# Kernel tuning notes

Hardware: AMD Instinct MI355X
Metric: run time of the kernel (lower is better)

Reference implementation:

```python
import jax, jax.numpy as jnp
import numpy as np

# model hyperparameters (from init_kwargs 'model' mapping)
SIG = 10.0       # kernel length scale
C = 0.0          # energy integration constant
STD = 1.0        # normalization std
M, N_ATOMS = 64, 24
T_ROWS, DESC = 6000, N_ATOMS * (N_ATOMS - 1) // 2  # 276


def setup_inputs() -> dict:
    key = jax.random.key(0)
    k1, k2, k3 = jax.random.split(key, 3)
    # spread atoms out so pairwise distances are O(1..10) Angstrom-like
    Rs = jax.random.normal(k1, (M, N_ATOMS, 3), jnp.float32) * 3.0
    # training descriptors are inverse distances -> positive values in (0,1)
    xs_train = jax.random.uniform(k2, (T_ROWS, DESC), jnp.float32)
    Jx_alphas = jax.random.normal(k3, (T_ROWS, DESC), jnp.float32) * 0.1
    return {"Rs": Rs, "xs_train": xs_train, "Jx_alphas": Jx_alphas}


def reference(Rs, xs_train, Jx_alphas):
    sig = SIG
    q = np.sqrt(5.0) / sig
    m, n = Rs.shape[0], Rs.shape[1]
    i, j = np.tril_indices(n, k=-1)  # lower-triangular atom pairs, P entries

    # pairwise coordinate differences [M, N, N, 3]
    diffs = Rs[:, :, None, :] - Rs[:, None, :, :]
    # inverse pairwise distances over tril pairs -> descriptor xs [M, P]
    d_ij = jnp.linalg.norm(diffs[:, i, j, :], axis=-1)
    xs = 1.0 / d_ij

    # descriptor differences to all (permuted) training points [M, T, P]
    x_diffs = q * xs[:, None, :] - q * xs_train[None, :, :]
    x_dists = jnp.linalg.norm(x_diffs, axis=-1)            # [M, T]
    exp_xs = (5.0 / (3.0 * sig ** 2)) * jnp.exp(-x_dists)  # [M, T]
    dot = jnp.einsum('mtp,tp->mt', x_diffs, Jx_alphas)     # [M, T]
    exp1 = exp_xs * (1.0 + x_dists)                        # [M, T]

    F1 = jnp.einsum('mt,mtp->mp', exp_xs * dot, x_diffs)   # [M, P]
    F2 = exp1 @ Jx_alphas                                  # [M, P]
    Fs_x = (F1 - F2) * xs ** 3                             # [M, P]

    # scatter pair forces back onto the symmetric [N, N] pair grid;
    # diagonal diffs are zero so leaving mult=0 there matches the original
    mult = jnp.zeros((m, n, n), Rs.dtype)
    mult = mult.at[:, i, j].set(Fs_x).at[:, j, i].set(Fs_x)
    Fs = (diffs * mult[..., None]).sum(axis=1) * STD       # [M, N, 3]

    Es = (exp1 * dot).sum(axis=-1) / q * STD + C           # [M]
    return Es, Fs
```

## Files before the change

kernel.cpp:

```cpp
#include <hip/hip_runtime.h>
#include <math.h>

#define MM 64
#define NA 24
#define NP 276
#define NT 6000
#define QC 0.22360679774997896f
#define EXPC 0.01666666666666667f

#define OFF_XS   0
#define OFF_UU   17664
#define OFF_VV   17728
#define OFF_C1   23728
#define OFF_ES   29728
#define OFF_SW   29792
#define OFF_SH   29856
#define OFF_WT   312480
#define OFF_ET   696480
#define ZTOT     282752

__device__ __forceinline__ float f4c(const float4& v, int i) {
  return i == 0 ? v.x : i == 1 ? v.y : i == 2 ? v.z : v.w;
}

__global__ __launch_bounds__(256) void k_pre(const float* __restrict__ Rs,
                                             const float* __restrict__ xt,
                                             const float* __restrict__ Ja,
                                             float* __restrict__ ws) {
  const int tid = threadIdx.x;
  for (int z = blockIdx.x * 256 + tid; z < ZTOT; z += gridDim.x * 256)
    ws[OFF_ES + z] = 0.f;

  if (blockIdx.x < MM) {
    const int m = blockIdx.x;
    __shared__ float sR[NA * 3];
    __shared__ float sAcc[4];
    if (tid < NA * 3) sR[tid] = Rs[m * NA * 3 + tid];
    __syncthreads();
    float acc = 0.f;
    for (int p = tid; p < NP; p += 256) {
      int i = (int)((1.0f + sqrtf(1.0f + 8.0f * (float)p)) * 0.5f);
      while (i * (i - 1) / 2 > p) i--;
      while ((i + 1) * i / 2 <= p) i++;
      int j = p - i * (i - 1) / 2;
      float dx = sR[i * 3 + 0] - sR[j * 3 + 0];
      float dy = sR[i * 3 + 1] - sR[j * 3 + 1];
      float dz = sR[i * 3 + 2] - sR[j * 3 + 2];
      float u = 1.0f / sqrtf(dx * dx + dy * dy + dz * dz);
      ws[OFF_XS + m * NP + p] = u;
      acc += u * u;
    }
    for (int off = 32; off; off >>= 1) acc += __shfl_down(acc, off);
    if ((tid & 63) == 0) sAcc[tid >> 6] = acc;
    __syncthreads();
    if (tid == 0) ws[OFF_UU + m] = sAcc[0] + sAcc[1] + sAcc[2] + sAcc[3];
  } else {
    const int t = (blockIdx.x - MM) * 4 + (tid >> 6);
    const int lane = tid & 63;
    if (t < NT) {
      const float* vrow = xt + (size_t)t * NP;
      const float* jrow = Ja + (size_t)t * NP;
      float a = 0.f, b = 0.f;
      for (int p = lane; p < NP; p += 64) {
        float v = vrow[p], j = jrow[p];
        a += v * v;
        b += v * j;
      }
      for (int off = 32; off; off >>= 1) {
        a += __shfl_down(a, off);
        b += __shfl_down(b, off);
      }
      if (lane == 0) { ws[OFF_VV + t] = a; ws[OFF_C1 + t] = b; }
    }
  }
}

#define G1_BS 278
__global__ __launch_bounds__(128) void k_g1(const float* __restrict__ xt,
                                            const float* __restrict__ Ja,
                                            float* __restrict__ ws) {
  __shared__ __align__(16) float2 Bs[16][G1_BS];
  const int tid = threadIdx.x;
  const int t0 = blockIdx.x * 16;
  const int my = blockIdx.y * 16;
  for (int idx = tid; idx < 16 * 69; idx += 128) {
    const int row = idx / 69;
    const int k = (idx - row * 69) * 4;
    const float4 v = *(const float4*)(xt + (size_t)(t0 + row) * NP + k);
    const float4 j = *(const float4*)(Ja + (size_t)(t0 + row) * NP + k);
    *(float4*)&Bs[row][k]     = make_float4(v.x, j.x, v.y, j.y);
    *(float4*)&Bs[row][k + 2] = make_float4(v.z, j.z, v.w, j.w);
  }
  const int r = tid >> 3;
  const int c = tid & 7;
  const int m = my + r;
  const float uum = ws[OFF_UU + m];
  const float2 vv2 = *(const float2*)(ws + OFF_VV + t0 + 2 * c);
  const float2 c12 = *(const float2*)(ws + OFF_C1 + t0 + 2 * c);
  const float* arow = ws + OFF_XS + m * NP;
  __syncthreads();

  float accv0 = 0.f, accj0 = 0.f, accv1 = 0.f, accj1 = 0.f;
#pragma unroll 3
  for (int k = 0; k < NP; k += 4) {
    const float4 a = *(const float4*)(arow + k);
    const float4 p00 = *(const float4*)&Bs[2 * c][k];
    const float4 p01 = *(const float4*)&Bs[2 * c][k + 2];
    const float4 p10 = *(const float4*)&Bs[2 * c + 1][k];
    const float4 p11 = *(const float4*)&Bs[2 * c + 1][k + 2];
    accv0 = fmaf(a.x, p00.x, accv0); accj0 = fmaf(a.x, p00.y, accj0);
    accv0 = fmaf(a.y, p00.z, accv0); accj0 = fmaf(a.y, p00.w, accj0);
    accv0 = fmaf(a.z, p01.x, accv0); accj0 = fmaf(a.z, p01.y, accj0);
    accv0 = fmaf(a.w, p01.z, accv0); accj0 = fmaf(a.w, p01.w, accj0);
    accv1 = fmaf(a.x, p10.x, accv1); accj1 = fmaf(a.x, p10.y, accj1);
    accv1 = fmaf(a.y, p10.z, accv1); accj1 = fmaf(a.y, p10.w, accj1);
    accv1 = fmaf(a.z, p11.x, accv1); accj1 = fmaf(a.z, p11.y, accj1);
    accv1 = fmaf(a.w, p11.z, accv1); accj1 = fmaf(a.w, p11.w, accj1);
  }

  float es_p = 0.f, sw_p = 0.f;
#pragma unroll
  for (int tt = 0; tt < 2; tt++) {
    const float g1v = tt ? accv1 : accv0;
    const float g2v = tt ? accj1 : accj0;
    const float vvt = tt ? vv2.y : vv2.x;
    const float c1t = tt ? c12.y : c12.x;
    float d2 = fmaxf(uum - 2.f * g1v + vvt, 0.f);
    float xd = QC * sqrtf(d2);
    float dv = QC * (g2v - c1t);
    float ex = EXPC * __expf(-xd);
    float e1v = ex * (1.f + xd);
    float w_ = ex * dv;
    const int t = t0 + 2 * c + tt;
    ws[OFF_WT + (size_t)t * 64 + m] = w_;
    ws[OFF_ET + (size_t)t * 64 + m] = e1v;
    es_p += e1v * dv;
    sw_p += w_;
  }
#pragma unroll
  for (int off = 4; off; off >>= 1) {
    es_p += __shfl_down(es_p, off);
    sw_p += __shfl_down(sw_p, off);
  }
  if (c == 0) {
    atomicAdd(ws + OFF_ES + m, es_p);
    atomicAdd(ws + OFF_SW + m, sw_p);
  }
}

#define G2_KC 125
__global__ __launch_bounds__(256) void k_g2(const float* __restrict__ xt,
                                            const float* __restrict__ Ja,
                                            float* __restrict__ ws) {
  __shared__ __align__(16) float Bsv[G2_KC][16];
  __shared__ __align__(16) float Bsj[G2_KC][16];
  const int tid = threadIdx.x;
  const int p0 = blockIdx.x * 16;
  const int k0 = blockIdx.y * G2_KC;
  const int validp = (NP - p0 < 16) ? (NP - p0) : 16;

  for (int idx = tid; idx < G2_KC * 8; idx += 256) {
    const int q = idx & 3;
    const int mat = (idx >> 2) & 1;
    const int row = idx >> 3;
    float4 val = make_float4(0.f, 0.f, 0.f, 0.f);
    if (q * 4 < validp)
      val = *(const float4*)((mat ? Ja : xt) + (size_t)(k0 + row) * NP + p0 + q * 4);
    *(float4*)&(mat ? Bsj : Bsv)[row][q * 4] = val;
  }
  __syncthreads();

  const int m = tid & 63;
  const int pg = tid >> 6;
  const float* wtp = ws + OFF_WT + (size_t)k0 * 64 + m;
  const float* etp = ws + OFF_ET + (size_t)k0 * 64 + m;
  float acc1[4] = {0.f, 0.f, 0.f, 0.f};
  float acc2[4] = {0.f, 0.f, 0.f, 0.f};

#pragma unroll 5
  for (int k = 0; k < G2_KC; k++) {
    const float aw = wtp[k * 64];
    const float ae = etp[k * 64];
    const float4 bv = *(const float4*)&Bsv[k][pg * 4];
    const float4 bj = *(const float4*)&Bsj[k][pg * 4];
    acc1[0] = fmaf(aw, bv.x, acc1[0]); acc2[0] = fmaf(ae, bj.x, acc2[0]);
    acc1[1] = fmaf(aw, bv.y, acc1[1]); acc2[1] = fmaf(ae, bj.y, acc2[1]);
    acc1[2] = fmaf(aw, bv.z, acc1[2]); acc2[2] = fmaf(ae, bj.z, acc2[2]);
    acc1[3] = fmaf(aw, bv.w, acc1[3]); acc2[3] = fmaf(ae, bj.w, acc2[3]);
  }

  const int sh = blockIdx.y & 7;
  float* base1 = ws + OFF_SH + (size_t)(sh * 2 + 0) * NP * 64;
  float* base2 = ws + OFF_SH + (size_t)(sh * 2 + 1) * NP * 64;
#pragma unroll
  for (int j = 0; j < 4; j++) {
    const int p = p0 + pg * 4 + j;
    if (p < NP && pg * 4 + j < validp) {
      atomicAdd(base1 + (size_t)p * 64 + m, acc1[j]);
      atomicAdd(base2 + (size_t)p * 64 + m, acc2[j]);
    }
  }
}

__global__ __launch_bounds__(320) void k_final(const float* __restrict__ Rs,
                                               const float* __restrict__ ws,
                                               float* __restrict__ out) {
  const int m = blockIdx.x;
  const int tid = threadIdx.x;
  __shared__ float fx[NP];
  __shared__ float sR[NA * 3];
  if (tid < NA * 3) sR[tid] = Rs[m * NA * 3 + tid];
  const float sw = ws[OFF_SW + m];
  for (int p = tid; p < NP; p += 320) {
    float f1p = 0.f, f2 = 0.f;
#pragma unroll
    for (int s = 0; s < 8; s++) {
      f1p += ws[OFF_SH + ((size_t)(s * 2 + 0) * NP + p) * 64 + m];
      f2  += ws[OFF_SH + ((size_t)(s * 2 + 1) * NP + p) * 64 + m];
    }
    const float u = ws[OFF_XS + m * NP + p];
    const float F1 = QC * (u * sw - f1p);
    fx[p] = (F1 - f2) * u * u * u;
  }
  __syncthreads();
  if (tid == 0) out[m] = ws[OFF_ES + m] / QC;
  if (tid < NA * 3) {
    const int a = tid / 3, cc = tid % 3;
    const float ra = sR[a * 3 + cc];
    float acc = 0.f;
    for (int b = 0; b < NA; b++) {
      if (b == a) continue;
      const int i = a > b ? a : b, j = a > b ? b : a;
      const int p = i * (i - 1) / 2 + j;
      acc += (sR[b * 3 + cc] - ra) * fx[p];
    }
    out[MM + m * NA * 3 + tid] = acc;
  }
}

extern "C" void kernel_launch(void* const* d_in, const int* in_sizes, int n_in,
                              void* d_out, int out_size, void* d_ws, size_t ws_size,
                              hipStream_t stream) {
  const float* Rs = (const float*)d_in[0];
  const float* xt = (const float*)d_in[1];
  const float* Ja = (const float*)d_in[2];
  float* out = (float*)d_out;
  float* ws = (float*)d_ws;

  k_pre<<<MM + NT / 4, 256, 0, stream>>>(Rs, xt, Ja, ws);
  k_g1<<<dim3(NT / 16, 4), 128, 0, stream>>>(xt, Ja, ws);
  k_g2<<<dim3(18, NT / G2_KC), 256, 0, stream>>>(xt, Ja, ws);
  k_final<<<MM, 320, 0, stream>>>(Rs, ws, out);
}
```

Measured before the change: 138.5 us.

## Transpose training data into interleaved p-major layout and restructure first GEMM

The preprocessing kernel now transposes xs_train and Jx_alphas into a p-major workspace buffer with interleaved (x, J) pairs, and stores the query descriptors p-major as well. The first distance/dot kernel is rewritten so each thread owns one training row and eight molecules, streaming coalesced float2 loads over p instead of staging tiles in shared memory. This is meant to remove the shared-memory tile loads and give coalesced global access with more register reuse. The cost is an extra full write and read of a transposed copy of the training data, plus fewer, smaller blocks in the first GEMM.

```diff
diff --git a/kernel.cpp b/kernel.cpp
--- a/kernel.cpp
+++ b/kernel.cpp
@@ -5,10 +5,11 @@
 #define NA 24
 #define NP 276
 #define NT 6000
+#define NTP 6016
 #define QC 0.22360679774997896f
 #define EXPC 0.01666666666666667f
 
-#define OFF_XS   0
+#define OFF_XST  0
 #define OFF_UU   17664
 #define OFF_VV   17728
 #define OFF_C1   23728
@@ -17,6 +18,7 @@
 #define OFF_SH   29856
 #define OFF_WT   312480
 #define OFF_ET   696480
+#define OFF_XJT  1080480
 #define ZTOT     282752
 
 __device__ __forceinline__ float f4c(const float4& v, int i) {
@@ -47,7 +49,7 @@
       float dy = sR[i * 3 + 1] - sR[j * 3 + 1];
       float dz = sR[i * 3 + 2] - sR[j * 3 + 2];
       float u = 1.0f / sqrtf(dx * dx + dy * dy + dz * dz);
-      ws[OFF_XS + m * NP + p] = u;
+      ws[OFF_XST + p * 64 + m] = u;
       acc += u * u;
     }
     for (int off = 32; off; off >>= 1) acc += __shfl_down(acc, off);
@@ -55,96 +57,123 @@
     __syncthreads();
     if (tid == 0) ws[OFF_UU + m] = sAcc[0] + sAcc[1] + sAcc[2] + sAcc[3];
   } else {
-    const int t = (blockIdx.x - MM) * 4 + (tid >> 6);
-    const int lane = tid & 63;
-    if (t < NT) {
-      const float* vrow = xt + (size_t)t * NP;
-      const float* jrow = Ja + (size_t)t * NP;
-      float a = 0.f, b = 0.f;
-      for (int p = lane; p < NP; p += 64) {
-        float v = vrow[p], j = jrow[p];
-        a += v * v;
-        b += v * j;
-      }
-      for (int off = 32; off; off >>= 1) {
-        a += __shfl_down(a, off);
-        b += __shfl_down(b, off);
-      }
-      if (lane == 0) { ws[OFF_VV + t] = a; ws[OFF_C1 + t] = b; }
-    }
-  }
-}
-
-#define G1_BS 278
-__global__ __launch_bounds__(128) void k_g1(const float* __restrict__ xt,
-                                            const float* __restrict__ Ja,
-                                            float* __restrict__ ws) {
-  __shared__ __align__(16) float2 Bs[16][G1_BS];
-  const int tid = threadIdx.x;
-  const int t0 = blockIdx.x * 16;
-  const int my = blockIdx.y * 16;
-  for (int idx = tid; idx < 16 * 69; idx += 128) {
-    const int row = idx / 69;
-    const int k = (idx - row * 69) * 4;
-    const float4 v = *(const float4*)(xt + (size_t)(t0 + row) * NP + k);
-    const float4 j = *(const float4*)(Ja + (size_t)(t0 + row) * NP + k);
-    *(float4*)&Bs[row][k]     = make_float4(v.x, j.x, v.y, j.y);
-    *(float4*)&Bs[row][k + 2] = make_float4(v.z, j.z, v.w, j.w);
-  }
-  const int r = tid >> 3;
-  const int c = tid & 7;
-  const int m = my + r;
-  const float uum = ws[OFF_UU + m];
-  const float2 vv2 = *(const float2*)(ws + OFF_VV + t0 + 2 * c);
-  const float2 c12 = *(const float2*)(ws + OFF_C1 + t0 + 2 * c);
-  const float* arow = ws + OFF_XS + m * NP;
-  __syncthreads();
-
-  float accv0 = 0.f, accj0 = 0.f, accv1 = 0.f, accj1 = 0.f;
-#pragma unroll 3
-  for (int k = 0; k < NP; k += 4) {
-    const float4 a = *(const float4*)(arow + k);
-    const float4 p00 = *(const float4*)&Bs[2 * c][k];
-    const float4 p01 = *(const float4*)&Bs[2 * c][k + 2];
-    const float4 p10 = *(const float4*)&Bs[2 * c + 1][k];
-    const float4 p11 = *(const float4*)&Bs[2 * c + 1][k + 2];
-    accv0 = fmaf(a.x, p00.x, accv0); accj0 = fmaf(a.x, p00.y, accj0);
-    accv0 = fmaf(a.y, p00.z, accv0); accj0 = fmaf(a.y, p00.w, accj0);
-    accv0 = fmaf(a.z, p01.x, accv0); accj0 = fmaf(a.z, p01.y, accj0);
-    accv0 = fmaf(a.w, p01.z, accv0); accj0 = fmaf(a.w, p01.w, accj0);
-    accv1 = fmaf(a.x, p10.x, accv1); accj1 = fmaf(a.x, p10.y, accj1);
-    accv1 = fmaf(a.y, p10.z, accv1); accj1 = fmaf(a.y, p10.w, accj1);
-    accv1 = fmaf(a.z, p11.x, accv1); accj1 = fmaf(a.z, p11.y, accj1);
-    accv1 = fmaf(a.w, p11.z, accv1); accj1 = fmaf(a.w, p11.w, accj1);
-  }
-
-  float es_p = 0.f, sw_p = 0.f;
-#pragma unroll
-  for (int tt = 0; tt < 2; tt++) {
-    const float g1v = tt ? accv1 : accv0;
-    const float g2v = tt ? accj1 : accj0;
-    const float vvt = tt ? vv2.y : vv2.x;
-    const float c1t = tt ? c12.y : c12.x;
-    float d2 = fmaxf(uum - 2.f * g1v + vvt, 0.f);
+    const int t0 = (blockIdx.x - MM) * 32;
+    const int tl = tid >> 5;
+    const int pl = tid & 31;
+    __shared__ float lx[32][33];
+    __shared__ float lj[32][33];
+    float vvp[4] = {0.f, 0.f, 0.f, 0.f};
+    float c1p[4] = {0.f, 0.f, 0.f, 0.f};
+    for (int c9 = 0; c9 < 9; c9++) {
+      const int p = c9 * 32 + pl;
+      const bool pok = (p < NP);
+      __syncthreads();
+#pragma unroll
+      for (int tt = 0; tt < 4; tt++) {
+        const int t = t0 + tl * 4 + tt;
+        float v = 0.f, j = 0.f;
+        if (pok && t < NT) {
+          v = xt[(size_t)t * NP + p];
+          j = Ja[(size_t)t * NP + p];
+        }
+        vvp[tt] += v * v;
+        c1p[tt] += v * j;
+        lx[pl][tl * 4 + tt] = v;
+        lj[pl][tl * 4 + tt] = j;
+      }
+      __syncthreads();
+      const int tlw = tid & 31;
+      const int plw = tid >> 5;
+#pragma unroll
+      for (int pp = 0; pp < 4; pp++) {
+        const int pLoc = plw * 4 + pp;
+        const int pOut = c9 * 32 + pLoc;
+        if (pOut < NP) {
+          *(float2*)(ws + OFF_XJT + ((size_t)pOut * NTP + t0 + tlw) * 2) =
+              make_float2(lx[pLoc][tlw], lj[pLoc][tlw]);
+        }
+      }
+    }
+#pragma unroll
+    for (int off = 16; off; off >>= 1) {
+#pragma unroll
+      for (int tt = 0; tt < 4; tt++) {
+        vvp[tt] += __shfl_down(vvp[tt], off, 32);
+        c1p[tt] += __shfl_down(c1p[tt], off, 32);
+      }
+    }
+    if (pl == 0) {
+#pragma unroll
+      for (int tt = 0; tt < 4; tt++) {
+        const int t = t0 + tl * 4 + tt;
+        if (t < NT) { ws[OFF_VV + t] = vvp[tt]; ws[OFF_C1 + t] = c1p[tt]; }
+      }
+    }
+  }
+}
+
+__global__ __launch_bounds__(64) void k_g1(float* __restrict__ ws) {
+  const int lane = threadIdx.x;
+  const int t = blockIdx.x * 64 + lane;
+  const int m0 = blockIdx.y * 8;
+  const float* __restrict__ xj = ws + OFF_XJT + (size_t)t * 2;
+  const float* __restrict__ xs = ws + OFF_XST + m0;
+  float av[8] = {0.f,0.f,0.f,0.f,0.f,0.f,0.f,0.f};
+  float aj[8] = {0.f,0.f,0.f,0.f,0.f,0.f,0.f,0.f};
+#pragma unroll 4
+  for (int p = 0; p < NP; p++) {
+    const float2 x = *(const float2*)(xj + (size_t)p * (NTP * 2));
+    const float4 a0 = *(const float4*)(xs + p * 64);
+    const float4 a1 = *(const float4*)(xs + p * 64 + 4);
+    av[0] = fmaf(a0.x, x.x, av[0]); aj[0] = fmaf(a0.x, x.y, aj[0]);
+    av[1] = fmaf(a0.y, x.x, av[1]); aj[1] = fmaf(a0.y, x.y, aj[1]);
+    av[2] = fmaf(a0.z, x.x, av[2]); aj[2] = fmaf(a0.z, x.y, aj[2]);
+    av[3] = fmaf(a0.w, x.x, av[3]); aj[3] = fmaf(a0.w, x.y, aj[3]);
+    av[4] = fmaf(a1.x, x.x, av[4]); aj[4] = fmaf(a1.x, x.y, aj[4]);
+    av[5] = fmaf(a1.y, x.x, av[5]); aj[5] = fmaf(a1.y, x.y, aj[5]);
+    av[6] = fmaf(a1.z, x.x, av[6]); aj[6] = fmaf(a1.z, x.y, aj[6]);
+    av[7] = fmaf(a1.w, x.x, av[7]); aj[7] = fmaf(a1.w, x.y, aj[7]);
+  }
+  const bool tok = (t < NT);
+  const float vvt = tok ? ws[OFF_VV + t] : 0.f;
+  const float c1t = tok ? ws[OFF_C1 + t] : 0.f;
+  float wv[8], ev[8], es8[8], sw8[8];
+#pragma unroll
+  for (int i = 0; i < 8; i++) {
+    const float uum = ws[OFF_UU + m0 + i];
+    float d2 = fmaxf(uum - 2.f * av[i] + vvt, 0.f);
     float xd = QC * sqrtf(d2);
-    float dv = QC * (g2v - c1t);
+    float dv = QC * (aj[i] - c1t);
     float ex = EXPC * __expf(-xd);
     float e1v = ex * (1.f + xd);
     float w_ = ex * dv;
-    const int t = t0 + 2 * c + tt;
-    ws[OFF_WT + (size_t)t * 64 + m] = w_;
-    ws[OFF_ET + (size_t)t * 64 + m] = e1v;
-    es_p += e1v * dv;
-    sw_p += w_;
-  }
-#pragma unroll
-  for (int off = 4; off; off >>= 1) {
-    es_p += __shfl_down(es_p, off);
-    sw_p += __shfl_down(sw_p, off);
-  }
-  if (c == 0) {
-    atomicAdd(ws + OFF_ES + m, es_p);
-    atomicAdd(ws + OFF_SW + m, sw_p);
+    if (!tok) { e1v = 0.f; w_ = 0.f; dv = 0.f; }
+    wv[i] = w_; ev[i] = e1v;
+    es8[i] = e1v * dv;
+    sw8[i] = w_;
+  }
+  if (tok) {
+    float* wp = ws + OFF_WT + (size_t)t * 64 + m0;
+    float* ep = ws + OFF_ET + (size_t)t * 64 + m0;
+    *(float4*)wp       = make_float4(wv[0], wv[1], wv[2], wv[3]);
+    *(float4*)(wp + 4) = make_float4(wv[4], wv[5], wv[6], wv[7]);
+    *(float4*)ep       = make_float4(ev[0], ev[1], ev[2], ev[3]);
+    *(float4*)(ep + 4) = make_float4(ev[4], ev[5], ev[6], ev[7]);
+  }
+#pragma unroll
+  for (int off = 32; off; off >>= 1) {
+#pragma unroll
+    for (int i = 0; i < 8; i++) {
+      es8[i] += __shfl_down(es8[i], off);
+      sw8[i] += __shfl_down(sw8[i], off);
+    }
+  }
+  if (lane == 0) {
+#pragma unroll
+    for (int i = 0; i < 8; i++) {
+      atomicAdd(ws + OFF_ES + m0 + i, es8[i]);
+      atomicAdd(ws + OFF_SW + m0 + i, sw8[i]);
+    }
   }
 }
 
@@ -218,7 +247,7 @@
       f1p += ws[OFF_SH + ((size_t)(s * 2 + 0) * NP + p) * 64 + m];
       f2  += ws[OFF_SH + ((size_t)(s * 2 + 1) * NP + p) * 64 + m];
     }
-    const float u = ws[OFF_XS + m * NP + p];
+    const float u = ws[OFF_XST + p * 64 + m];
     const float F1 = QC * (u * sw - f1p);
     fx[p] = (F1 - f2) * u * u * u;
   }
@@ -247,8 +276,8 @@
   float* out = (float*)d_out;
   float* ws = (float*)d_ws;
 
-  k_pre<<<MM + NT / 4, 256, 0, stream>>>(Rs, xt, Ja, ws);
-  k_g1<<<dim3(NT / 16, 4), 128, 0, stream>>>(xt, Ja, ws);
+  k_pre<<<MM + 188, 256, 0, stream>>>(Rs, xt, Ja, ws);
+  k_g1<<<dim3(94, 8), 64, 0, stream>>>(ws);
   k_g2<<<dim3(18, NT / G2_KC), 256, 0, stream>>>(xt, Ja, ws);
   k_final<<<MM, 320, 0, stream>>>(Rs, ws, out);
 }
```

Result: slower. 175.5 us (+26.7%).

## Register-block k_g1 over four molecules and split k_g2 into independent accumulation chains

Applied to the files above, without the earlier changes.

k_g1 now computes all 64 molecules per block, with each thread handling 4 molecules by 2 training rows. This lets one shared-memory tile of training data be reused across all molecules instead of being reloaded by four blocks. Results are written as float4 stores, and the per-molecule energy sums are reduced in shared memory before one atomic per molecule. k_g2 moves to a 128-row K chunk (47 chunks, with the workspace tail zero-padded) and splits accumulation into four interleaved chains to expose more memory-level and FMA parallelism. The trade-offs are higher register pressure, fewer k_g1 blocks, and a slightly shifted workspace layout.

```diff
diff --git a/kernel.cpp b/kernel.cpp
--- a/kernel.cpp
+++ b/kernel.cpp
@@ -5,6 +5,7 @@
 #define NA 24
 #define NP 276
 #define NT 6000
+#define NTP 6016
 #define QC 0.22360679774997896f
 #define EXPC 0.01666666666666667f
 
@@ -16,7 +17,7 @@
 #define OFF_SW   29792
 #define OFF_SH   29856
 #define OFF_WT   312480
-#define OFF_ET   696480
+#define OFF_ET   697504
 #define ZTOT     282752
 
 __device__ __forceinline__ float f4c(const float4& v, int i) {
@@ -30,6 +31,10 @@
   const int tid = threadIdx.x;
   for (int z = blockIdx.x * 256 + tid; z < ZTOT; z += gridDim.x * 256)
     ws[OFF_ES + z] = 0.f;
+  for (int z = blockIdx.x * 256 + tid; z < 2048; z += gridDim.x * 256) {
+    if (z < 1024) ws[OFF_WT + 384000 + z] = 0.f;
+    else         ws[OFF_ET + 384000 + (z - 1024)] = 0.f;
+  }
 
   if (blockIdx.x < MM) {
     const int m = blockIdx.x;
@@ -80,9 +85,9 @@
                                             const float* __restrict__ Ja,
                                             float* __restrict__ ws) {
   __shared__ __align__(16) float2 Bs[16][G1_BS];
+  __shared__ float sEs[64], sSw[64];
   const int tid = threadIdx.x;
   const int t0 = blockIdx.x * 16;
-  const int my = blockIdx.y * 16;
   for (int idx = tid; idx < 16 * 69; idx += 128) {
     const int row = idx / 69;
     const int k = (idx - row * 69) * 4;
@@ -91,64 +96,92 @@
     *(float4*)&Bs[row][k]     = make_float4(v.x, j.x, v.y, j.y);
     *(float4*)&Bs[row][k + 2] = make_float4(v.z, j.z, v.w, j.w);
   }
+  const int c = tid & 7;
   const int r = tid >> 3;
-  const int c = tid & 7;
-  const int m = my + r;
-  const float uum = ws[OFF_UU + m];
+  const float* __restrict__ ar0 = ws + OFF_XS + (4 * r + 0) * NP;
+  const float* __restrict__ ar1 = ws + OFF_XS + (4 * r + 1) * NP;
+  const float* __restrict__ ar2 = ws + OFF_XS + (4 * r + 2) * NP;
+  const float* __restrict__ ar3 = ws + OFF_XS + (4 * r + 3) * NP;
+  const float4 uu4 = *(const float4*)(ws + OFF_UU + 4 * r);
   const float2 vv2 = *(const float2*)(ws + OFF_VV + t0 + 2 * c);
   const float2 c12 = *(const float2*)(ws + OFF_C1 + t0 + 2 * c);
-  const float* arow = ws + OFF_XS + m * NP;
-  __syncthreads();
-
-  float accv0 = 0.f, accj0 = 0.f, accv1 = 0.f, accj1 = 0.f;
+  __syncthreads();
+
+  float accv[2][4] = {{0.f,0.f,0.f,0.f},{0.f,0.f,0.f,0.f}};
+  float accj[2][4] = {{0.f,0.f,0.f,0.f},{0.f,0.f,0.f,0.f}};
 #pragma unroll 3
-  for (int k = 0; k < NP; k += 4) {
-    const float4 a = *(const float4*)(arow + k);
-    const float4 p00 = *(const float4*)&Bs[2 * c][k];
-    const float4 p01 = *(const float4*)&Bs[2 * c][k + 2];
-    const float4 p10 = *(const float4*)&Bs[2 * c + 1][k];
-    const float4 p11 = *(const float4*)&Bs[2 * c + 1][k + 2];
-    accv0 = fmaf(a.x, p00.x, accv0); accj0 = fmaf(a.x, p00.y, accj0);
-    accv0 = fmaf(a.y, p00.z, accv0); accj0 = fmaf(a.y, p00.w, accj0);
-    accv0 = fmaf(a.z, p01.x, accv0); accj0 = fmaf(a.z, p01.y, accj0);
-    accv0 = fmaf(a.w, p01.z, accv0); accj0 = fmaf(a.w, p01.w, accj0);
-    accv1 = fmaf(a.x, p10.x, accv1); accj1 = fmaf(a.x, p10.y, accj1);
-    accv1 = fmaf(a.y, p10.z, accv1); accj1 = fmaf(a.y, p10.w, accj1);
-    accv1 = fmaf(a.z, p11.x, accv1); accj1 = fmaf(a.z, p11.y, accj1);
-    accv1 = fmaf(a.w, p11.z, accv1); accj1 = fmaf(a.w, p11.w, accj1);
-  }
-
-  float es_p = 0.f, sw_p = 0.f;
+  for (int q = 0; q < 69; q++) {
+    const int k = 4 * q;
+    float4 A[4];
+    A[0] = *(const float4*)(ar0 + k);
+    A[1] = *(const float4*)(ar1 + k);
+    A[2] = *(const float4*)(ar2 + k);
+    A[3] = *(const float4*)(ar3 + k);
+    const float4 b00 = *(const float4*)&Bs[2 * c][k];
+    const float4 b01 = *(const float4*)&Bs[2 * c][k + 2];
+    const float4 b10 = *(const float4*)&Bs[2 * c + 1][k];
+    const float4 b11 = *(const float4*)&Bs[2 * c + 1][k + 2];
+#pragma unroll
+    for (int i = 0; i < 4; i++) {
+      const float4 a = A[i];
+      accv[0][i] = fmaf(a.x, b00.x, accv[0][i]); accj[0][i] = fmaf(a.x, b00.y, accj[0][i]);
+      accv[0][i] = fmaf(a.y, b00.z, accv[0][i]); accj[0][i] = fmaf(a.y, b00.w, accj[0][i]);
+      accv[0][i] = fmaf(a.z, b01.x, accv[0][i]); accj[0][i] = fmaf(a.z, b01.y, accj[0][i]);
+      accv[0][i] = fmaf(a.w, b01.z, accv[0][i]); accj[0][i] = fmaf(a.w, b01.w, accj[0][i]);
+      accv[1][i] = fmaf(a.x, b10.x, accv[1][i]); accj[1][i] = fmaf(a.x, b10.y, accj[1][i]);
+      accv[1][i] = fmaf(a.y, b10.z, accv[1][i]); accj[1][i] = fmaf(a.y, b10.w, accj[1][i]);
+      accv[1][i] = fmaf(a.z, b11.x, accv[1][i]); accj[1][i] = fmaf(a.z, b11.y, accj[1][i]);
+      accv[1][i] = fmaf(a.w, b11.z, accv[1][i]); accj[1][i] = fmaf(a.w, b11.w, accj[1][i]);
+    }
+  }
+
+  float es_p[4] = {0.f,0.f,0.f,0.f}, sw_p[4] = {0.f,0.f,0.f,0.f};
+  float wv[2][4], ev[2][4];
 #pragma unroll
   for (int tt = 0; tt < 2; tt++) {
-    const float g1v = tt ? accv1 : accv0;
-    const float g2v = tt ? accj1 : accj0;
     const float vvt = tt ? vv2.y : vv2.x;
     const float c1t = tt ? c12.y : c12.x;
-    float d2 = fmaxf(uum - 2.f * g1v + vvt, 0.f);
-    float xd = QC * sqrtf(d2);
-    float dv = QC * (g2v - c1t);
-    float ex = EXPC * __expf(-xd);
-    float e1v = ex * (1.f + xd);
-    float w_ = ex * dv;
+#pragma unroll
+    for (int i = 0; i < 4; i++) {
+      float d2 = fmaxf(f4c(uu4, i) - 2.f * accv[tt][i] + vvt, 0.f);
+      float xd = QC * sqrtf(d2);
+      float dv = QC * (accj[tt][i] - c1t);
+      float ex = EXPC * __expf(-xd);
+      float e1v = ex * (1.f + xd);
+      float w_ = ex * dv;
+      wv[tt][i] = w_; ev[tt][i] = e1v;
+      es_p[i] += e1v * dv;
+      sw_p[i] += w_;
+    }
+  }
+#pragma unroll
+  for (int tt = 0; tt < 2; tt++) {
     const int t = t0 + 2 * c + tt;
-    ws[OFF_WT + (size_t)t * 64 + m] = w_;
-    ws[OFF_ET + (size_t)t * 64 + m] = e1v;
-    es_p += e1v * dv;
-    sw_p += w_;
+    *(float4*)(ws + OFF_WT + (size_t)t * 64 + 4 * r) =
+        make_float4(wv[tt][0], wv[tt][1], wv[tt][2], wv[tt][3]);
+    *(float4*)(ws + OFF_ET + (size_t)t * 64 + 4 * r) =
+        make_float4(ev[tt][0], ev[tt][1], ev[tt][2], ev[tt][3]);
   }
 #pragma unroll
   for (int off = 4; off; off >>= 1) {
-    es_p += __shfl_down(es_p, off);
-    sw_p += __shfl_down(sw_p, off);
+#pragma unroll
+    for (int i = 0; i < 4; i++) {
+      es_p[i] += __shfl_down(es_p[i], off, 8);
+      sw_p[i] += __shfl_down(sw_p[i], off, 8);
+    }
   }
   if (c == 0) {
-    atomicAdd(ws + OFF_ES + m, es_p);
-    atomicAdd(ws + OFF_SW + m, sw_p);
-  }
-}
-
-#define G2_KC 125
+#pragma unroll
+    for (int i = 0; i < 4; i++) { sEs[4 * r + i] = es_p[i]; sSw[4 * r + i] = sw_p[i]; }
+  }
+  __syncthreads();
+  if (tid < 64) {
+    atomicAdd(ws + OFF_ES + tid, sEs[tid]);
+    atomicAdd(ws + OFF_SW + tid, sSw[tid]);
+  }
+}
+
+#define G2_KC 128
 __global__ __launch_bounds__(256) void k_g2(const float* __restrict__ xt,
                                             const float* __restrict__ Ja,
                                             float* __restrict__ ws) {
@@ -164,7 +197,7 @@
     const int mat = (idx >> 2) & 1;
     const int row = idx >> 3;
     float4 val = make_float4(0.f, 0.f, 0.f, 0.f);
-    if (q * 4 < validp)
+    if (q * 4 < validp && k0 + row < NT)
       val = *(const float4*)((mat ? Ja : xt) + (size_t)(k0 + row) * NP + p0 + q * 4);
     *(float4*)&(mat ? Bsj : Bsv)[row][q * 4] = val;
   }
@@ -172,21 +205,29 @@
 
   const int m = tid & 63;
   const int pg = tid >> 6;
-  const float* wtp = ws + OFF_WT + (size_t)k0 * 64 + m;
-  const float* etp = ws + OFF_ET + (size_t)k0 * 64 + m;
-  float acc1[4] = {0.f, 0.f, 0.f, 0.f};
-  float acc2[4] = {0.f, 0.f, 0.f, 0.f};
-
-#pragma unroll 5
-  for (int k = 0; k < G2_KC; k++) {
-    const float aw = wtp[k * 64];
-    const float ae = etp[k * 64];
-    const float4 bv = *(const float4*)&Bsv[k][pg * 4];
-    const float4 bj = *(const float4*)&Bsj[k][pg * 4];
-    acc1[0] = fmaf(aw, bv.x, acc1[0]); acc2[0] = fmaf(ae, bj.x, acc2[0]);
-    acc1[1] = fmaf(aw, bv.y, acc1[1]); acc2[1] = fmaf(ae, bj.y, acc2[1]);
-    acc1[2] = fmaf(aw, bv.z, acc1[2]); acc2[2] = fmaf(ae, bj.z, acc2[2]);
-    acc1[3] = fmaf(aw, bv.w, acc1[3]); acc2[3] = fmaf(ae, bj.w, acc2[3]);
+  const float* __restrict__ wtp = ws + OFF_WT + (size_t)k0 * 64 + m;
+  const float* __restrict__ etp = ws + OFF_ET + (size_t)k0 * 64 + m;
+  float acc1[4][4] = {{0}}, acc2[4][4] = {{0}};
+
+#pragma unroll 2
+  for (int i = 0; i < 32; i++) {
+    float aw[4], ae[4];
+#pragma unroll
+    for (int s = 0; s < 4; s++) {
+      const int k = 32 * s + i;
+      aw[s] = wtp[k * 64];
+      ae[s] = etp[k * 64];
+    }
+#pragma unroll
+    for (int s = 0; s < 4; s++) {
+      const int k = 32 * s + i;
+      const float4 bv = *(const float4*)&Bsv[k][pg * 4];
+      const float4 bj = *(const float4*)&Bsj[k][pg * 4];
+      acc1[s][0] = fmaf(aw[s], bv.x, acc1[s][0]); acc2[s][0] = fmaf(ae[s], bj.x, acc2[s][0]);
+      acc1[s][1] = fmaf(aw[s], bv.y, acc1[s][1]); acc2[s][1] = fmaf(ae[s], bj.y, acc2[s][1]);
+      acc1[s][2] = fmaf(aw[s], bv.z, acc1[s][2]); acc2[s][2] = fmaf(ae[s], bj.z, acc2[s][2]);
+      acc1[s][3] = fmaf(aw[s], bv.w, acc1[s][3]); acc2[s][3] = fmaf(ae[s], bj.w, acc2[s][3]);
+    }
   }
 
   const int sh = blockIdx.y & 7;
@@ -195,9 +236,11 @@
 #pragma unroll
   for (int j = 0; j < 4; j++) {
     const int p = p0 + pg * 4 + j;
-    if (p < NP && pg * 4 + j < validp) {
-      atomicAdd(base1 + (size_t)p * 64 + m, acc1[j]);
-      atomicAdd(base2 + (size_t)p * 64 + m, acc2[j]);
+    if (pg * 4 + j < validp) {
+      const float v1 = acc1[0][j] + acc1[1][j] + acc1[2][j] + acc1[3][j];
+      const float v2 = acc2[0][j] + acc2[1][j] + acc2[2][j] + acc2[3][j];
+      atomicAdd(base1 + (size_t)p * 64 + m, v1);
+      atomicAdd(base2 + (size_t)p * 64 + m, v2);
     }
   }
 }
@@ -248,7 +291,7 @@
   float* ws = (float*)d_ws;
 
   k_pre<<<MM + NT / 4, 256, 0, stream>>>(Rs, xt, Ja, ws);
-  k_g1<<<dim3(NT / 16, 4), 128, 0, stream>>>(xt, Ja, ws);
-  k_g2<<<dim3(18, NT / G2_KC), 256, 0, stream>>>(xt, Ja, ws);
+  k_g1<<<NT / 16, 128, 0, stream>>>(xt, Ja, ws);
+  k_g2<<<dim3(18, 47), 256, 0, stream>>>(xt, Ja, ws);
   k_final<<<MM, 320, 0, stream>>>(Rs, ws, out);
 }
```

New measurement: 144.6 us. +4.4%, slower.

## Stage operands in LDS with register tiling and fold row norms into g1

Applied to the files above, without the earlier changes.

The per-training-row norms are now computed inside k_g1 from tiles already loaded into shared memory, so k_pre no longer reads the training matrices. The descriptor matrix is stored transposed, and k_g1 stages 32 molecules per block in LDS using a 2x2 register tile with block-level reductions before its atomics. k_g2 stages the W/E tiles in LDS and uses a 2x2 outer-product tile with padded K=96 chunks, and the workspace tail is zeroed to cover that padding. The aim is less redundant global traffic and fewer uncoalesced loads, at the cost of more LDS use and extra synchronisation.

```diff
diff --git a/kernel.cpp b/kernel.cpp
--- a/kernel.cpp
+++ b/kernel.cpp
@@ -5,18 +5,17 @@
 #define NA 24
 #define NP 276
 #define NT 6000
+#define NTP 6048
 #define QC 0.22360679774997896f
 #define EXPC 0.01666666666666667f
 
-#define OFF_XS   0
+#define OFF_XST  0
 #define OFF_UU   17664
-#define OFF_VV   17728
-#define OFF_C1   23728
-#define OFF_ES   29728
-#define OFF_SW   29792
-#define OFF_SH   29856
-#define OFF_WT   312480
-#define OFF_ET   696480
+#define OFF_ES   17728
+#define OFF_SW   17792
+#define OFF_SH   17856
+#define OFF_WT   300480
+#define OFF_ET   687552
 #define ZTOT     282752
 
 __device__ __forceinline__ float f4c(const float4& v, int i) {
@@ -24,13 +23,14 @@
 }
 
 __global__ __launch_bounds__(256) void k_pre(const float* __restrict__ Rs,
-                                             const float* __restrict__ xt,
-                                             const float* __restrict__ Ja,
                                              float* __restrict__ ws) {
   const int tid = threadIdx.x;
   for (int z = blockIdx.x * 256 + tid; z < ZTOT; z += gridDim.x * 256)
     ws[OFF_ES + z] = 0.f;
-
+  for (int z = blockIdx.x * 256 + tid; z < 6144; z += gridDim.x * 256) {
+    if (z < 3072) ws[OFF_WT + 384000 + z] = 0.f;
+    else          ws[OFF_ET + 384000 + (z - 3072)] = 0.f;
+  }
   if (blockIdx.x < MM) {
     const int m = blockIdx.x;
     __shared__ float sR[NA * 3];
@@ -47,157 +47,180 @@
       float dy = sR[i * 3 + 1] - sR[j * 3 + 1];
       float dz = sR[i * 3 + 2] - sR[j * 3 + 2];
       float u = 1.0f / sqrtf(dx * dx + dy * dy + dz * dz);
-      ws[OFF_XS + m * NP + p] = u;
+      ws[OFF_XST + p * 64 + m] = u;
       acc += u * u;
     }
     for (int off = 32; off; off >>= 1) acc += __shfl_down(acc, off);
     if ((tid & 63) == 0) sAcc[tid >> 6] = acc;
     __syncthreads();
     if (tid == 0) ws[OFF_UU + m] = sAcc[0] + sAcc[1] + sAcc[2] + sAcc[3];
-  } else {
-    const int t = (blockIdx.x - MM) * 4 + (tid >> 6);
-    const int lane = tid & 63;
-    if (t < NT) {
-      const float* vrow = xt + (size_t)t * NP;
-      const float* jrow = Ja + (size_t)t * NP;
-      float a = 0.f, b = 0.f;
-      for (int p = lane; p < NP; p += 64) {
-        float v = vrow[p], j = jrow[p];
-        a += v * v;
-        b += v * j;
-      }
-      for (int off = 32; off; off >>= 1) {
-        a += __shfl_down(a, off);
-        b += __shfl_down(b, off);
-      }
-      if (lane == 0) { ws[OFF_VV + t] = a; ws[OFF_C1 + t] = b; }
-    }
-  }
-}
-
-#define G1_BS 278
-__global__ __launch_bounds__(128) void k_g1(const float* __restrict__ xt,
-                                            const float* __restrict__ Ja,
-                                            float* __restrict__ ws) {
+  }
+}
+
+#define G1_BS 280
+#define G1_AS 36
+__global__ __launch_bounds__(256, 2) void k_g1(const float* __restrict__ xt,
+                                               const float* __restrict__ Ja,
+                                               float* __restrict__ ws) {
   __shared__ __align__(16) float2 Bs[16][G1_BS];
+  __shared__ __align__(16) float As[NP][G1_AS];
+  __shared__ float sVV[16], sC1[16];
+  __shared__ float sEsW[4][32], sSwW[4][32];
   const int tid = threadIdx.x;
   const int t0 = blockIdx.x * 16;
-  const int my = blockIdx.y * 16;
-  for (int idx = tid; idx < 16 * 69; idx += 128) {
+  const int m0 = blockIdx.y * 32;
+
+  for (int idx = tid; idx < 16 * 69; idx += 256) {
     const int row = idx / 69;
-    const int k = (idx - row * 69) * 4;
-    const float4 v = *(const float4*)(xt + (size_t)(t0 + row) * NP + k);
-    const float4 j = *(const float4*)(Ja + (size_t)(t0 + row) * NP + k);
-    *(float4*)&Bs[row][k]     = make_float4(v.x, j.x, v.y, j.y);
-    *(float4*)&Bs[row][k + 2] = make_float4(v.z, j.z, v.w, j.w);
-  }
-  const int r = tid >> 3;
-  const int c = tid & 7;
-  const int m = my + r;
-  const float uum = ws[OFF_UU + m];
-  const float2 vv2 = *(const float2*)(ws + OFF_VV + t0 + 2 * c);
-  const float2 c12 = *(const float2*)(ws + OFF_C1 + t0 + 2 * c);
-  const float* arow = ws + OFF_XS + m * NP;
-  __syncthreads();
-
-  float accv0 = 0.f, accj0 = 0.f, accv1 = 0.f, accj1 = 0.f;
-#pragma unroll 3
-  for (int k = 0; k < NP; k += 4) {
-    const float4 a = *(const float4*)(arow + k);
-    const float4 p00 = *(const float4*)&Bs[2 * c][k];
-    const float4 p01 = *(const float4*)&Bs[2 * c][k + 2];
-    const float4 p10 = *(const float4*)&Bs[2 * c + 1][k];
-    const float4 p11 = *(const float4*)&Bs[2 * c + 1][k + 2];
-    accv0 = fmaf(a.x, p00.x, accv0); accj0 = fmaf(a.x, p00.y, accj0);
-    accv0 = fmaf(a.y, p00.z, accv0); accj0 = fmaf(a.y, p00.w, accj0);
-    accv0 = fmaf(a.z, p01.x, accv0); accj0 = fmaf(a.z, p01.y, accj0);
-    accv0 = fmaf(a.w, p01.z, accv0); accj0 = fmaf(a.w, p01.w, accj0);
-    accv1 = fmaf(a.x, p10.x, accv1); accj1 = fmaf(a.x, p10.y, accj1);
-    accv1 = fmaf(a.y, p10.z, accv1); accj1 = fmaf(a.y, p10.w, accj1);
-    accv1 = fmaf(a.z, p11.x, accv1); accj1 = fmaf(a.z, p11.y, accj1);
-    accv1 = fmaf(a.w, p11.z, accv1); accj1 = fmaf(a.w, p11.w, accj1);
-  }
-
-  float es_p = 0.f, sw_p = 0.f;
-#pragma unroll
-  for (int tt = 0; tt < 2; tt++) {
-    const float g1v = tt ? accv1 : accv0;
-    const float g2v = tt ? accj1 : accj0;
-    const float vvt = tt ? vv2.y : vv2.x;
-    const float c1t = tt ? c12.y : c12.x;
+    const int kq = (idx - row * 69) * 4;
+    const float4 v = *(const float4*)(xt + (size_t)(t0 + row) * NP + kq);
+    const float4 j = *(const float4*)(Ja + (size_t)(t0 + row) * NP + kq);
+    *(float4*)&Bs[row][kq]     = make_float4(v.x, j.x, v.y, j.y);
+    *(float4*)&Bs[row][kq + 2] = make_float4(v.z, j.z, v.w, j.w);
+  }
+  for (int idx = tid; idx < NP * 8; idx += 256) {
+    const int p = idx >> 3;
+    const int mq = (idx & 7) * 4;
+    *(float4*)&As[p][mq] = *(const float4*)(ws + OFF_XST + p * 64 + m0 + mq);
+  }
+  const int r = tid & 15;
+  const int c = tid >> 4;
+  const float2 uu2 = *(const float2*)(ws + OFF_UU + m0 + 2 * r);
+  __syncthreads();
+
+  {
+    const int tl = tid >> 4;
+    const int l16 = tid & 15;
+    float a = 0.f, b = 0.f;
+    for (int k = l16; k < NP; k += 16) {
+      const float2 x = Bs[tl][k];
+      a = fmaf(x.x, x.x, a);
+      b = fmaf(x.x, x.y, b);
+    }
+#pragma unroll
+    for (int off = 8; off; off >>= 1) {
+      a += __shfl_down(a, off, 16);
+      b += __shfl_down(b, off, 16);
+    }
+    if (l16 == 0) { sVV[tl] = a; sC1[tl] = b; }
+  }
+  __syncthreads();
+
+  float av0 = 0.f, av1 = 0.f, aj0 = 0.f, aj1 = 0.f;
+#pragma unroll 4
+  for (int kk = 0; kk < NP; kk += 2) {
+    const float4 b  = *(const float4*)&Bs[c][kk];
+    const float2 a0 = *(const float2*)&As[kk][2 * r];
+    const float2 a1 = *(const float2*)&As[kk + 1][2 * r];
+    av0 = fmaf(a0.x, b.x, av0); aj0 = fmaf(a0.x, b.y, aj0);
+    av1 = fmaf(a0.y, b.x, av1); aj1 = fmaf(a0.y, b.y, aj1);
+    av0 = fmaf(a1.x, b.z, av0); aj0 = fmaf(a1.x, b.w, aj0);
+    av1 = fmaf(a1.y, b.z, av1); aj1 = fmaf(a1.y, b.w, aj1);
+  }
+
+  const float vvt = sVV[c];
+  const float c1t = sC1[c];
+  float es2[2], sw2[2], wv[2], ev[2];
+#pragma unroll
+  for (int i = 0; i < 2; i++) {
+    const float g1v = i ? av1 : av0;
+    const float g2v = i ? aj1 : aj0;
+    const float uum = i ? uu2.y : uu2.x;
     float d2 = fmaxf(uum - 2.f * g1v + vvt, 0.f);
     float xd = QC * sqrtf(d2);
     float dv = QC * (g2v - c1t);
     float ex = EXPC * __expf(-xd);
     float e1v = ex * (1.f + xd);
     float w_ = ex * dv;
-    const int t = t0 + 2 * c + tt;
-    ws[OFF_WT + (size_t)t * 64 + m] = w_;
-    ws[OFF_ET + (size_t)t * 64 + m] = e1v;
-    es_p += e1v * dv;
-    sw_p += w_;
-  }
-#pragma unroll
-  for (int off = 4; off; off >>= 1) {
-    es_p += __shfl_down(es_p, off);
-    sw_p += __shfl_down(sw_p, off);
-  }
-  if (c == 0) {
-    atomicAdd(ws + OFF_ES + m, es_p);
-    atomicAdd(ws + OFF_SW + m, sw_p);
-  }
-}
-
-#define G2_KC 125
-__global__ __launch_bounds__(256) void k_g2(const float* __restrict__ xt,
-                                            const float* __restrict__ Ja,
-                                            float* __restrict__ ws) {
-  __shared__ __align__(16) float Bsv[G2_KC][16];
-  __shared__ __align__(16) float Bsj[G2_KC][16];
+    wv[i] = w_; ev[i] = e1v;
+    es2[i] = e1v * dv;
+    sw2[i] = w_;
+  }
+  const int t = t0 + c;
+  *(float2*)(ws + OFF_WT + (size_t)t * 64 + m0 + 2 * r) = make_float2(wv[0], wv[1]);
+  *(float2*)(ws + OFF_ET + (size_t)t * 64 + m0 + 2 * r) = make_float2(ev[0], ev[1]);
+
+#pragma unroll
+  for (int i = 0; i < 2; i++) {
+    es2[i] += __shfl_down(es2[i], 32); es2[i] += __shfl_down(es2[i], 16);
+    sw2[i] += __shfl_down(sw2[i], 32); sw2[i] += __shfl_down(sw2[i], 16);
+  }
+  const int w = tid >> 6;
+  if ((tid & 63) < 16) {
+    sEsW[w][2 * r + 0] = es2[0]; sEsW[w][2 * r + 1] = es2[1];
+    sSwW[w][2 * r + 0] = sw2[0]; sSwW[w][2 * r + 1] = sw2[1];
+  }
+  __syncthreads();
+  if (tid < 32) {
+    const float es = sEsW[0][tid] + sEsW[1][tid] + sEsW[2][tid] + sEsW[3][tid];
+    const float sw = sSwW[0][tid] + sSwW[1][tid] + sSwW[2][tid] + sSwW[3][tid];
+    atomicAdd(ws + OFF_ES + m0 + tid, es);
+    atomicAdd(ws + OFF_SW + m0 + tid, sw);
+  }
+}
+
+#define G2_KC 96
+#define G2_AS 68
+#define G2_BS 18
+__global__ __launch_bounds__(256, 2) void k_g2(const float* __restrict__ xt,
+                                               const float* __restrict__ Ja,
+                                               float* __restrict__ ws) {
+  __shared__ __align__(16) float Aw[G2_KC][G2_AS];
+  __shared__ __align__(16) float Ae[G2_KC][G2_AS];
+  __shared__ __align__(16) float2 Bvj[G2_KC][G2_BS];
   const int tid = threadIdx.x;
   const int p0 = blockIdx.x * 16;
   const int k0 = blockIdx.y * G2_KC;
   const int validp = (NP - p0 < 16) ? (NP - p0) : 16;
 
-  for (int idx = tid; idx < G2_KC * 8; idx += 256) {
-    const int q = idx & 3;
-    const int mat = (idx >> 2) & 1;
-    const int row = idx >> 3;
-    float4 val = make_float4(0.f, 0.f, 0.f, 0.f);
-    if (q * 4 < validp)
-      val = *(const float4*)((mat ? Ja : xt) + (size_t)(k0 + row) * NP + p0 + q * 4);
-    *(float4*)&(mat ? Bsj : Bsv)[row][q * 4] = val;
-  }
-  __syncthreads();
-
-  const int m = tid & 63;
-  const int pg = tid >> 6;
-  const float* wtp = ws + OFF_WT + (size_t)k0 * 64 + m;
-  const float* etp = ws + OFF_ET + (size_t)k0 * 64 + m;
-  float acc1[4] = {0.f, 0.f, 0.f, 0.f};
-  float acc2[4] = {0.f, 0.f, 0.f, 0.f};
-
-#pragma unroll 5
+  for (int idx = tid; idx < G2_KC * 16; idx += 256) {
+    const int k = idx >> 4;
+    const int mq = (idx & 15) * 4;
+    *(float4*)&Aw[k][mq] = *(const float4*)(ws + OFF_WT + (size_t)(k0 + k) * 64 + mq);
+    *(float4*)&Ae[k][mq] = *(const float4*)(ws + OFF_ET + (size_t)(k0 + k) * 64 + mq);
+  }
+  for (int idx = tid; idx < G2_KC * 4; idx += 256) {
+    const int k = idx >> 2;
+    const int pq = (idx & 3) * 4;
+    const int t = k0 + k;
+    float4 v = make_float4(0.f, 0.f, 0.f, 0.f), j = v;
+    if (pq < validp && t < NT) {
+      v = *(const float4*)(xt + (size_t)t * NP + p0 + pq);
+      j = *(const float4*)(Ja + (size_t)t * NP + p0 + pq);
+    }
+    *(float4*)&Bvj[k][pq]     = make_float4(v.x, j.x, v.y, j.y);
+    *(float4*)&Bvj[k][pq + 2] = make_float4(v.z, j.z, v.w, j.w);
+  }
+  __syncthreads();
+
+  const int r = tid & 31;
+  const int c = tid >> 5;
+  float f1[2][2] = {{0.f, 0.f}, {0.f, 0.f}};
+  float f2[2][2] = {{0.f, 0.f}, {0.f, 0.f}};
+#pragma unroll 4
   for (int k = 0; k < G2_KC; k++) {
-    const float aw = wtp[k * 64];
-    const float ae = etp[k * 64];
-    const float4 bv = *(const float4*)&Bsv[k][pg * 4];
-    const float4 bj = *(const float4*)&Bsj[k][pg * 4];
-    acc1[0] = fmaf(aw, bv.x, acc1[0]); acc2[0] = fmaf(ae, bj.x, acc2[0]);
-    acc1[1] = fmaf(aw, bv.y, acc1[1]); acc2[1] = fmaf(ae, bj.y, acc2[1]);
-    acc1[2] = fmaf(aw, bv.z, acc1[2]); acc2[2] = fmaf(ae, bj.z, acc2[2]);
-    acc1[3] = fmaf(aw, bv.w, acc1[3]); acc2[3] = fmaf(ae, bj.w, acc2[3]);
+    const float2 aw = *(const float2*)&Aw[k][2 * r];
+    const float2 ae = *(const float2*)&Ae[k][2 * r];
+    const float4 b  = *(const float4*)&Bvj[k][2 * c];
+    f1[0][0] = fmaf(aw.x, b.x, f1[0][0]); f1[0][1] = fmaf(aw.x, b.z, f1[0][1]);
+    f1[1][0] = fmaf(aw.y, b.x, f1[1][0]); f1[1][1] = fmaf(aw.y, b.z, f1[1][1]);
+    f2[0][0] = fmaf(ae.x, b.y, f2[0][0]); f2[0][1] = fmaf(ae.x, b.w, f2[0][1]);
+    f2[1][0] = fmaf(ae.y, b.y, f2[1][0]); f2[1][1] = fmaf(ae.y, b.w, f2[1][1]);
   }
 
   const int sh = blockIdx.y & 7;
-  float* base1 = ws + OFF_SH + (size_t)(sh * 2 + 0) * NP * 64;
-  float* base2 = ws + OFF_SH + (size_t)(sh * 2 + 1) * NP * 64;
-#pragma unroll
-  for (int j = 0; j < 4; j++) {
-    const int p = p0 + pg * 4 + j;
-    if (p < NP && pg * 4 + j < validp) {
-      atomicAdd(base1 + (size_t)p * 64 + m, acc1[j]);
-      atomicAdd(base2 + (size_t)p * 64 + m, acc2[j]);
+  float* b1 = ws + OFF_SH + (size_t)(sh * 2 + 0) * NP * 64;
+  float* b2 = ws + OFF_SH + (size_t)(sh * 2 + 1) * NP * 64;
+#pragma unroll
+  for (int j = 0; j < 2; j++) {
+    const int pl = 2 * c + j;
+    if (pl < validp) {
+      const int p = p0 + pl;
+#pragma unroll
+      for (int i = 0; i < 2; i++) {
+        atomicAdd(b1 + (size_t)p * 64 + 2 * r + i, f1[i][j]);
+        atomicAdd(b2 + (size_t)p * 64 + 2 * r + i, f2[i][j]);
+      }
     }
   }
 }
@@ -218,7 +241,7 @@
       f1p += ws[OFF_SH + ((size_t)(s * 2 + 0) * NP + p) * 64 + m];
       f2  += ws[OFF_SH + ((size_t)(s * 2 + 1) * NP + p) * 64 + m];
     }
-    const float u = ws[OFF_XS + m * NP + p];
+    const float u = ws[OFF_XST + p * 64 + m];
     const float F1 = QC * (u * sw - f1p);
     fx[p] = (F1 - f2) * u * u * u;
   }
@@ -247,8 +270,8 @@
   float* out = (float*)d_out;
   float* ws = (float*)d_ws;
 
-  k_pre<<<MM + NT / 4, 256, 0, stream>>>(Rs, xt, Ja, ws);
-  k_g1<<<dim3(NT / 16, 4), 128, 0, stream>>>(xt, Ja, ws);
-  k_g2<<<dim3(18, NT / G2_KC), 256, 0, stream>>>(xt, Ja, ws);
+  k_pre<<<256, 256, 0, stream>>>(Rs, ws);
+  k_g1<<<dim3(375, 2), 256, 0, stream>>>(xt, Ja, ws);
+  k_g2<<<dim3(18, 63), 256, 0, stream>>>(xt, Ja, ws);
   k_final<<<MM, 320, 0, stream>>>(Rs, ws, out);
 }
```

Result: no change. 136.2 us (-1.7%).
